# Optimization experiments

Hardware: AMD Instinct MI355X
Metric: run time of the kernel (lower is better)

The kernel has to match this reference:

```python
import jax, jax.numpy as jnp
import numpy as np

KH = KW = 3
SH = SW = 1
DH = DW = 1

def _same_padding(ih, iw):
    eff_kh = (KH - 1) * DH + 1
    eff_kw = (KW - 1) * DW + 1
    out_h = (ih + SH - 1) // SH
    out_w = (iw + SW - 1) // SW
    pad_h = max((out_h - 1) * SH + eff_kh - ih, 0)
    pad_w = max((out_w - 1) * SW + eff_kw - iw, 0)
    pad_top = pad_h // 2
    pad_bottom = pad_h - pad_top
    pad_left = pad_w // 2
    pad_right = pad_w - pad_left
    return (pad_top, pad_bottom), (pad_left, pad_right)


def setup_inputs() -> dict:
    key = jax.random.key(0)
    k1, k2, k3 = jax.random.split(key, 3)
    N, C, H, Wd = 32, 192, 56, 56
    Cout = 384
    x = jax.random.normal(k1, (N, C, H, Wd), dtype=jnp.float32)
    # linear weight (Cout, C*KH*KW) with unfold ordering (c, kh, kw) -> OIHW kernel
    W = jax.random.normal(k2, (Cout, C, KH, KW), dtype=jnp.float32) * (1.0 / np.sqrt(C * KH * KW))
    b = jax.random.normal(k3, (Cout,), dtype=jnp.float32) * 0.01
    return {"x": x, "W": W, "b": b}


def reference(x, W, b):
    # ConvLayer: F.pad('same') -> nn.Unfold -> Linear -> reshape, which is
    # mathematically a 2D conv with OIHW kernel W (unfold orders features as c,kh,kw).
    _, _, H, Wd = x.shape
    pad_hw = _same_padding(H, Wd)
    out = jax.lax.conv_general_dilated(
        x, W,
        window_strides=(SH, SW),
        padding=pad_hw,
        rhs_dilation=(DH, DW),
        dimension_numbers=("NCHW", "OIHW", "NCHW"),
    )
    return out + b[None, :, None, None]
```

## Files before the change

### kernel.cpp

```cpp
#include <hip/hip_runtime.h>
#include <cstdint>
#include <cstddef>

#define N_IMG 32
#define C_IN 192
#define HW 56
#define SPAT 3136
#define C_OUT 384
#define HP 58
#define KPOS 9
#define KTOT 1728
#define NPH 54

#define BM 128
#define BN 256
#define NT_CO 3
#define NT_S  392
#define GRID_MAIN (NT_CO*NT_S)

#define BUF_EL 12288
#define B_BASE 4096

typedef __attribute__((ext_vector_type(8))) short short8;
typedef __attribute__((ext_vector_type(4))) float f32x4;

__device__ __forceinline__ unsigned short f2bf(float f) {
  union { float f; unsigned u; } v; v.f = f;
  unsigned u = v.u;
  unsigned r = (u + 0x7FFFu + ((u >> 16) & 1u)) >> 16;
  return (unsigned short)r;
}

__device__ __forceinline__ void async_load16(const void* gsrc, void* ldst) {
  __builtin_amdgcn_global_load_lds(
      (const __attribute__((address_space(1))) unsigned int*)gsrc,
      (__attribute__((address_space(3))) unsigned int*)ldst,
      16, 0, 0);
}

__device__ __forceinline__ void vm3() { asm volatile("s_waitcnt vmcnt(3)" ::: "memory"); }
__device__ __forceinline__ void vm0() { asm volatile("s_waitcnt vmcnt(0)" ::: "memory"); }
#define SBAR0() __builtin_amdgcn_sched_barrier(0)

__global__ void pack_w(const float* __restrict__ W, unsigned short* __restrict__ Wp) {
  int idx = blockIdx.x*256 + threadIdx.x;
  if (idx >= C_OUT*KPOS*C_IN) return;
  int c   = idx % C_IN;
  int pos = (idx / C_IN) % KPOS;
  int co  = idx / (C_IN*KPOS);
  float v = W[((size_t)co*C_IN + c)*KPOS + pos];
  Wp[idx] = f2bf(v);
}

__global__ void zero_border(unsigned short* __restrict__ Xp) {
  int idx = blockIdx.x*256 + threadIdx.x;
  if (idx >= N_IMG*228*C_IN) return;
  int c    = idx % C_IN;
  int cell = (idx / C_IN) % 228;
  int n    = idx / (C_IN*228);
  int hh, ww;
  if (cell < 116) { hh = (cell < 58) ? 0 : 57; ww = cell % 58; }
  else { int b2 = cell - 116; ww = (b2 < 56) ? 0 : 57; hh = 1 + (b2 % 56); }
  Xp[(((size_t)n*HP + hh)*HP + ww)*C_IN + c] = 0;
}

__global__ void pack_x(const float* __restrict__ x, unsigned short* __restrict__ Xp) {
  __shared__ float tile[64*57];
  int b  = blockIdx.x;
  int cb = b % 3;
  int h  = (b/3) % HW;
  int n  = b / (3*HW);
  int tid = threadIdx.x;
  const float* src = x + (size_t)n*C_IN*SPAT + (size_t)cb*64*SPAT + h*HW;
  #pragma unroll
  for (int i = 0; i < 14; ++i) {
    int idx = i*256 + tid;
    int c = idx / HW, w = idx % HW;
    tile[c*57 + w] = src[(size_t)c*SPAT + w];
  }
  __syncthreads();
  unsigned short* dst = Xp + (((size_t)n*HP + h + 1)*HP + 1)*C_IN + cb*64;
  #pragma unroll
  for (int i = 0; i < 14; ++i) {
    int idx = i*256 + tid;
    int w = idx / 64, c = idx % 64;
    dst[(size_t)w*C_IN + c] = f2bf(tile[c*57 + w]);
  }
}

__global__ __launch_bounds__(512, 4) void conv_gemm(
    const unsigned short* __restrict__ Wp,
    const unsigned short* __restrict__ Xp,
    const float* __restrict__ bias,
    float* __restrict__ out)
{
  __shared__ __attribute__((aligned(16))) unsigned short lds[3][BUF_EL];

  int bid = blockIdx.x;
  int wg = (bid & 7) * (GRID_MAIN/8) + (bid >> 3);
  int cotile = wg % NT_CO;
  int stile  = wg / NT_CO;

  const int tid   = threadIdx.x;
  const int lane  = tid & 63;
  const int wv    = tid >> 6;
  const int wm    = wv >> 2;
  const int wn    = wv & 3;
  const int lanep = lane & 15;
  const int laneq = lane >> 4;
  const int r4    = (lane >> 2) & 15;
  const int c4    = lane & 3;
  const int gsl   = (c4 ^ ((r4 >> 1) & 3)) << 3;

  const unsigned short* aSrc = Wp + (size_t)(cotile*BM + wv*16 + r4)*KTOT + gsl;
  const unsigned short* bSrc0;
  const unsigned short* bSrc1;
  {
    int f0 = stile*BN + (wv*2 + 0)*16 + r4;
    int n0 = f0 / SPAT, sp0 = f0 % SPAT;
    bSrc0 = Xp + (((size_t)n0*HP + sp0/HW)*HP + sp0%HW)*C_IN + gsl;
    int f1 = stile*BN + (wv*2 + 1)*16 + r4;
    int n1 = f1 / SPAT, sp1 = f1 % SPAT;
    bSrc1 = Xp + (((size_t)n1*HP + sp1/HW)*HP + sp1%HW)*C_IN + gsl;
  }

  const int rsw = (laneq ^ ((lanep >> 1) & 3)) << 3;
  const int aRd = (wm*64 + lanep)*32 + rsw;
  const int bRd = B_BASE + (wn*64 + lanep)*32 + rsw;

  f32x4 acc[4][4];
  #pragma unroll
  for (int mf = 0; mf < 4; ++mf)
    #pragma unroll
    for (int nf = 0; nf < 4; ++nf)
      acc[mf][nf] = (f32x4){0.f, 0.f, 0.f, 0.f};

  auto stage = [&](int t, unsigned short* base) {
    int pos = t / 6;
    int c0  = (t - pos*6) * 32;
    int kh  = pos / 3, kw = pos - kh*3;
    int bo  = (kh*HP + kw)*C_IN + c0;
    async_load16(aSrc + t*32, base + wv*512);
    async_load16(bSrc0 + bo, base + B_BASE + (wv*2 + 0)*512);
    async_load16(bSrc1 + bo, base + B_BASE + (wv*2 + 1)*512);
  };

#define PHASE(LB, STAGE_STMT, VM_STMT, DO_BAR)                              \
  {                                                                         \
    const unsigned short* lb_ = (LB);                                       \
    short8 av_[4], bv_[4];                                                  \
    _Pragma("unroll")                                                       \
    for (int mf = 0; mf < 4; ++mf) av_[mf] = *(const short8*)&lb_[aRd + mf*512]; \
    _Pragma("unroll")                                                       \
    for (int nf = 0; nf < 4; ++nf) bv_[nf] = *(const short8*)&lb_[bRd + nf*512]; \
    STAGE_STMT;                                                             \
    __builtin_amdgcn_s_setprio(1);                                          \
    _Pragma("unroll")                                                       \
    for (int mf = 0; mf < 4; ++mf)                                          \
      _Pragma("unroll")                                                     \
      for (int nf = 0; nf < 4; ++nf)                                        \
        acc[mf][nf] = __builtin_amdgcn_mfma_f32_16x16x32_bf16(              \
            av_[mf], bv_[nf], acc[mf][nf], 0, 0, 0);                        \
    __builtin_amdgcn_s_setprio(0);                                          \
    VM_STMT;                                                                \
    if (DO_BAR) {                                                           \
      __builtin_amdgcn_s_barrier();                                         \
      SBAR0();                                                              \
    }                                                                       \
  }

  unsigned short* b0 = &lds[0][0];
  unsigned short* b1 = &lds[1][0];
  unsigned short* b2 = &lds[2][0];

  stage(0, b0);
  stage(1, b1);
  vm3();
  __builtin_amdgcn_s_barrier();
  SBAR0();

  for (int t0 = 0; t0 < 51; t0 += 3) {
    PHASE(b0, (stage(t0 + 2, b2)), vm3(), true);
    PHASE(b1, (stage(t0 + 3, b0)), vm3(), true);
    PHASE(b2, (stage(t0 + 4, b1)), vm3(), true);
  }
  PHASE(b0, (stage(53, b2)), vm3(), true);
  PHASE(b1, (void)0, vm0(), true);
  PHASE(b2, (void)0, (void)0, false);
#undef PHASE

  const int coB = cotile*BM + wm*64;
  const int fB  = stile*BN + wn*64;
  #pragma unroll
  for (int nf = 0; nf < 4; ++nf) {
    int f  = fB + nf*16 + lanep;
    int n  = f / SPAT;
    int sp = f % SPAT;
    float* obase = out + (size_t)n*C_OUT*SPAT + sp;
    #pragma unroll
    for (int mf = 0; mf < 4; ++mf) {
      #pragma unroll
      for (int i = 0; i < 4; ++i) {
        int co = coB + mf*16 + laneq*4 + i;
        obase[(size_t)co*SPAT] = acc[mf][nf][i] + bias[co];
      }
    }
  }
}

__global__ void conv_naive(const float* __restrict__ x, const float* __restrict__ W,
                           const float* __restrict__ bias, float* __restrict__ out) {
  size_t idx = (size_t)blockIdx.x*256 + threadIdx.x;
  if (idx >= (size_t)N_IMG*C_OUT*SPAT) return;
  int s  = idx % SPAT;
  int co = (int)((idx / SPAT) % C_OUT);
  int n  = (int)(idx / ((size_t)SPAT*C_OUT));
  int h = s / HW, w = s % HW;
  float acc = bias[co];
  for (int c = 0; c < C_IN; ++c)
    for (int kh = 0; kh < 3; ++kh) {
      int hh = h + kh - 1;
      if (hh < 0 || hh >= HW) continue;
      for (int kw = 0; kw < 3; ++kw) {
        int ww = w + kw - 1;
        if (ww < 0 || ww >= HW) continue;
        acc += x[(((size_t)n*C_IN + c)*HW + hh)*HW + ww]
             * W[(((size_t)co*C_IN + c)*3 + kh)*3 + kw];
      }
    }
  out[idx] = acc;
}

extern "C" void kernel_launch(void* const* d_in, const int* in_sizes, int n_in,
                              void* d_out, int out_size, void* d_ws, size_t ws_size,
                              hipStream_t stream) {
  const float* x = (const float*)d_in[0];
  const float* W = (const float*)d_in[1];
  const float* b = (const float*)d_in[2];
  float* out = (float*)d_out;

  const size_t WP_ELEMS = (size_t)C_OUT*KTOT;
  const size_t XP_ELEMS = (size_t)N_IMG*HP*HP*C_IN;
  const size_t NEED = (WP_ELEMS + XP_ELEMS)*2;

  if (ws_size >= NEED) {
    unsigned short* Wp = (unsigned short*)d_ws;
    unsigned short* Xp = Wp + WP_ELEMS;
    zero_border<<<(N_IMG*228*C_IN + 255)/256, 256, 0, stream>>>(Xp);
    pack_w<<<(int)((WP_ELEMS + 255)/256), 256, 0, stream>>>(W, Wp);
    pack_x<<<N_IMG*HW*3, 256, 0, stream>>>(x, Xp);
    conv_gemm<<<GRID_MAIN, 512, 0, stream>>>(Wp, Xp, b, out);
  } else {
    size_t total = (size_t)N_IMG*C_OUT*SPAT;
    conv_naive<<<(int)((total + 255)/256), 256, 0, stream>>>(x, W, b, out);
  }
}
```

Before: 172.2 us.

## Use persistent 4-wave blocks with 128x64 warp tiles in conv GEMM

The conv GEMM now launches a fixed grid of 1024 blocks of 256 threads. Each block loops persistently over the 1176 output tiles, and each wave computes a 128x64 sub-tile (8x4 MFMA fragments) instead of 64x64 with 8 waves. Each wave issues six async loads per stage, so the waitcnt threshold rises to vmcnt(6), and a trailing barrier protects LDS reuse across tiles. The goal is more MFMA work per LDS read and less launch and tail imbalance. The cost is roughly double the accumulator registers, lower occupancy, and an uneven tile count per block (1176 over 1024).

```diff
diff --git a/kernel.cpp b/kernel.cpp
--- a/kernel.cpp
+++ b/kernel.cpp
@@ -16,7 +16,8 @@
 #define BN 256
 #define NT_CO 3
 #define NT_S  392
-#define GRID_MAIN (NT_CO*NT_S)
+#define NT_ALL (NT_CO*NT_S)
+#define GRID_MAIN 1024
 
 #define BUF_EL 12288
 #define B_BASE 4096
@@ -38,7 +39,7 @@
       16, 0, 0);
 }
 
-__device__ __forceinline__ void vm3() { asm volatile("s_waitcnt vmcnt(3)" ::: "memory"); }
+__device__ __forceinline__ void vm6() { asm volatile("s_waitcnt vmcnt(6)" ::: "memory"); }
 __device__ __forceinline__ void vm0() { asm volatile("s_waitcnt vmcnt(0)" ::: "memory"); }
 #define SBAR0() __builtin_amdgcn_sched_barrier(0)
 
@@ -88,7 +89,7 @@
   }
 }
 
-__global__ __launch_bounds__(512, 4) void conv_gemm(
+__global__ __launch_bounds__(256, 2) void conv_gemm(
     const unsigned short* __restrict__ Wp,
     const unsigned short* __restrict__ Xp,
     const float* __restrict__ bias,
@@ -98,111 +99,111 @@
 
   int bid = blockIdx.x;
   int wg = (bid & 7) * (GRID_MAIN/8) + (bid >> 3);
-  int cotile = wg % NT_CO;
-  int stile  = wg / NT_CO;
 
   const int tid   = threadIdx.x;
   const int lane  = tid & 63;
   const int wv    = tid >> 6;
-  const int wm    = wv >> 2;
-  const int wn    = wv & 3;
   const int lanep = lane & 15;
   const int laneq = lane >> 4;
   const int r4    = (lane >> 2) & 15;
   const int c4    = lane & 3;
   const int gsl   = (c4 ^ ((r4 >> 1) & 3)) << 3;
-
-  const unsigned short* aSrc = Wp + (size_t)(cotile*BM + wv*16 + r4)*KTOT + gsl;
-  const unsigned short* bSrc0;
-  const unsigned short* bSrc1;
-  {
-    int f0 = stile*BN + (wv*2 + 0)*16 + r4;
-    int n0 = f0 / SPAT, sp0 = f0 % SPAT;
-    bSrc0 = Xp + (((size_t)n0*HP + sp0/HW)*HP + sp0%HW)*C_IN + gsl;
-    int f1 = stile*BN + (wv*2 + 1)*16 + r4;
-    int n1 = f1 / SPAT, sp1 = f1 % SPAT;
-    bSrc1 = Xp + (((size_t)n1*HP + sp1/HW)*HP + sp1%HW)*C_IN + gsl;
-  }
-
-  const int rsw = (laneq ^ ((lanep >> 1) & 3)) << 3;
-  const int aRd = (wm*64 + lanep)*32 + rsw;
-  const int bRd = B_BASE + (wn*64 + lanep)*32 + rsw;
-
-  f32x4 acc[4][4];
-  #pragma unroll
-  for (int mf = 0; mf < 4; ++mf)
-    #pragma unroll
-    for (int nf = 0; nf < 4; ++nf)
-      acc[mf][nf] = (f32x4){0.f, 0.f, 0.f, 0.f};
-
-  auto stage = [&](int t, unsigned short* base) {
-    int pos = t / 6;
-    int c0  = (t - pos*6) * 32;
-    int kh  = pos / 3, kw = pos - kh*3;
-    int bo  = (kh*HP + kw)*C_IN + c0;
-    async_load16(aSrc + t*32, base + wv*512);
-    async_load16(bSrc0 + bo, base + B_BASE + (wv*2 + 0)*512);
-    async_load16(bSrc1 + bo, base + B_BASE + (wv*2 + 1)*512);
-  };
-
-#define PHASE(LB, STAGE_STMT, VM_STMT, DO_BAR)                              \
-  {                                                                         \
-    const unsigned short* lb_ = (LB);                                       \
-    short8 av_[4], bv_[4];                                                  \
-    _Pragma("unroll")                                                       \
-    for (int mf = 0; mf < 4; ++mf) av_[mf] = *(const short8*)&lb_[aRd + mf*512]; \
-    _Pragma("unroll")                                                       \
-    for (int nf = 0; nf < 4; ++nf) bv_[nf] = *(const short8*)&lb_[bRd + nf*512]; \
-    STAGE_STMT;                                                             \
-    __builtin_amdgcn_s_setprio(1);                                          \
-    _Pragma("unroll")                                                       \
-    for (int mf = 0; mf < 4; ++mf)                                          \
-      _Pragma("unroll")                                                     \
-      for (int nf = 0; nf < 4; ++nf)                                        \
-        acc[mf][nf] = __builtin_amdgcn_mfma_f32_16x16x32_bf16(              \
-            av_[mf], bv_[nf], acc[mf][nf], 0, 0, 0);                        \
-    __builtin_amdgcn_s_setprio(0);                                          \
-    VM_STMT;                                                                \
-    if (DO_BAR) {                                                           \
-      __builtin_amdgcn_s_barrier();                                         \
-      SBAR0();                                                              \
-    }                                                                       \
-  }
+  const int rsw   = (laneq ^ ((lanep >> 1) & 3)) << 3;
 
   unsigned short* b0 = &lds[0][0];
   unsigned short* b1 = &lds[1][0];
   unsigned short* b2 = &lds[2][0];
 
-  stage(0, b0);
-  stage(1, b1);
-  vm3();
-  __builtin_amdgcn_s_barrier();
-  SBAR0();
-
-  for (int t0 = 0; t0 < 51; t0 += 3) {
-    PHASE(b0, (stage(t0 + 2, b2)), vm3(), true);
-    PHASE(b1, (stage(t0 + 3, b0)), vm3(), true);
-    PHASE(b2, (stage(t0 + 4, b1)), vm3(), true);
-  }
-  PHASE(b0, (stage(53, b2)), vm3(), true);
-  PHASE(b1, (void)0, vm0(), true);
-  PHASE(b2, (void)0, (void)0, false);
+  for (int tt = wg; tt < NT_ALL; tt += GRID_MAIN) {
+    const int cotile = tt % NT_CO;
+    const int stile  = tt / NT_CO;
+
+    const unsigned short* aSrc0 = Wp + (size_t)(cotile*BM + wv*16     + r4)*KTOT + gsl;
+    const unsigned short* aSrc1 = Wp + (size_t)(cotile*BM + (wv+4)*16 + r4)*KTOT + gsl;
+    const unsigned short* bSrc[4];
+    #pragma unroll
+    for (int i = 0; i < 4; ++i) {
+      int f  = stile*BN + (wv*4 + i)*16 + r4;
+      int n  = f / SPAT, sp = f % SPAT;
+      bSrc[i] = Xp + (((size_t)n*HP + sp/HW)*HP + sp%HW)*C_IN + gsl;
+    }
+
+    f32x4 acc[8][4];
+    #pragma unroll
+    for (int mf = 0; mf < 8; ++mf)
+      #pragma unroll
+      for (int nf = 0; nf < 4; ++nf)
+        acc[mf][nf] = (f32x4){0.f, 0.f, 0.f, 0.f};
+
+    auto stage = [&](int t, unsigned short* base) {
+      int pos = t / 6;
+      int c0  = (t - pos*6) * 32;
+      int kh  = pos / 3, kw = pos - kh*3;
+      int bo  = (kh*HP + kw)*C_IN + c0;
+      async_load16(aSrc0 + t*32, base + wv*512);
+      async_load16(aSrc1 + t*32, base + (wv+4)*512);
+      #pragma unroll
+      for (int i = 0; i < 4; ++i)
+        async_load16(bSrc[i] + bo, base + B_BASE + (wv*4 + i)*512);
+    };
+
+#define PHASE(LB, STAGE_STMT, VM_STMT, DO_BAR)                              \
+    {                                                                       \
+      const unsigned short* lb_ = (LB);                                     \
+      short8 av_[8], bv_[4];                                                \
+      _Pragma("unroll")                                                     \
+      for (int mf = 0; mf < 8; ++mf)                                        \
+        av_[mf] = *(const short8*)&lb_[(mf*16 + lanep)*32 + rsw];           \
+      _Pragma("unroll")                                                     \
+      for (int nf = 0; nf < 4; ++nf)                                        \
+        bv_[nf] = *(const short8*)&lb_[B_BASE + (wv*64 + nf*16 + lanep)*32 + rsw]; \
+      STAGE_STMT;                                                           \
+      __builtin_amdgcn_s_setprio(1);                                        \
+      _Pragma("unroll")                                                     \
+      for (int mf = 0; mf < 8; ++mf)                                        \
+        _Pragma("unroll")                                                   \
+        for (int nf = 0; nf < 4; ++nf)                                      \
+          acc[mf][nf] = __builtin_amdgcn_mfma_f32_16x16x32_bf16(            \
+              av_[mf], bv_[nf], acc[mf][nf], 0, 0, 0);                      \
+      __builtin_amdgcn_s_setprio(0);                                        \
+      VM_STMT;                                                              \
+      if (DO_BAR) {                                                         \
+        __builtin_amdgcn_s_barrier();                                       \
+        SBAR0();                                                            \
+      }                                                                     \
+    }
+
+    stage(0, b0);
+    stage(1, b1);
+    vm6();
+    __builtin_amdgcn_s_barrier();
+    SBAR0();
+
+    for (int t0 = 0; t0 < 51; t0 += 3) {
+      PHASE(b0, (stage(t0 + 2, b2)), vm6(), true);
+      PHASE(b1, (stage(t0 + 3, b0)), vm6(), true);
+      PHASE(b2, (stage(t0 + 4, b1)), vm6(), true);
+    }
+    PHASE(b0, (stage(53, b2)), vm6(), true);
+    PHASE(b1, (void)0, vm0(), true);
+    PHASE(b2, (void)0, (void)0, true);
 #undef PHASE
 
-  const int coB = cotile*BM + wm*64;
-  const int fB  = stile*BN + wn*64;
-  #pragma unroll
-  for (int nf = 0; nf < 4; ++nf) {
-    int f  = fB + nf*16 + lanep;
-    int n  = f / SPAT;
-    int sp = f % SPAT;
-    float* obase = out + (size_t)n*C_OUT*SPAT + sp;
+    const int coB = cotile*BM;
+    const int fB  = stile*BN + wv*64;
     #pragma unroll
-    for (int mf = 0; mf < 4; ++mf) {
+    for (int nf = 0; nf < 4; ++nf) {
+      int f  = fB + nf*16 + lanep;
+      int n  = f / SPAT;
+      int sp = f % SPAT;
+      float* obase = out + (size_t)n*C_OUT*SPAT + sp;
       #pragma unroll
-      for (int i = 0; i < 4; ++i) {
-        int co = coB + mf*16 + laneq*4 + i;
-        obase[(size_t)co*SPAT] = acc[mf][nf][i] + bias[co];
+      for (int mf = 0; mf < 8; ++mf) {
+        #pragma unroll
+        for (int i = 0; i < 4; ++i) {
+          int co = coB + mf*16 + laneq*4 + i;
+          obase[(size_t)co*SPAT] = acc[mf][nf][i] + bias[co];
+        }
       }
     }
   }
@@ -249,7 +250,7 @@
     zero_border<<<(N_IMG*228*C_IN + 255)/256, 256, 0, stream>>>(Xp);
     pack_w<<<(int)((WP_ELEMS + 255)/256), 256, 0, stream>>>(W, Wp);
     pack_x<<<N_IMG*HW*3, 256, 0, stream>>>(x, Xp);
-    conv_gemm<<<GRID_MAIN, 512, 0, stream>>>(Wp, Xp, b, out);
+    conv_gemm<<<GRID_MAIN, 256, 0, stream>>>(Wp, Xp, b, out);
   } else {
     size_t total = (size_t)N_IMG*C_OUT*SPAT;
     conv_naive<<<(int)((total + 255)/256), 256, 0, stream>>>(x, W, b, out);
```

After: 251.5 us. +46.0%, slower.
